# Performance work log

Hardware: AMD Instinct MI355X
Metric: run time of the kernel (lower is better)

The kernel has to match this reference:

```python
import jax, jax.numpy as jnp
import numpy as np

B = 131072      # batch
IN = 1024       # input_dim
H = 384         # hidden[0]
L = 128         # latent_dim = hidden[1]
K = 32          # slots_k
R = 2           # top_r
TAU = 0.7


def setup_inputs() -> dict:
    key = jax.random.key(0)
    ks = jax.random.split(key, 8)
    s = 0.02
    f32 = jnp.float32
    return {
        "x":  jax.random.normal(ks[0], (B, IN), f32),
        "w1": jax.random.normal(ks[1], (IN, H), f32) * s,
        "b1": jnp.zeros((H,), f32),
        "w2": jax.random.normal(ks[2], (H, L), f32) * s,
        "b2": jnp.zeros((L,), f32),
        "mk": jax.random.normal(ks[3], (K, L), f32) * s,  # memory_keys
        "mv": jax.random.normal(ks[4], (K, L), f32) * s,  # memory_values
        "w3": jax.random.normal(ks[5], (2 * L, H), f32) * s,
        "b3": jnp.zeros((H,), f32),
        "w4": jax.random.normal(ks[6], (H, 1), f32) * s,
        "b4": jnp.zeros((1,), f32),
    }


def reference(x, w1, b1, w2, b2, mk, mv, w3, b3, w4, b4):
    # block_a: Linear -> GELU -> (Dropout=id in eval) -> Linear -> GELU
    z = jax.nn.gelu(x @ w1 + b1, approximate=False)
    z = jax.nn.gelu(z @ w2 + b2, approximate=False)          # [B, L]

    # top-r slot attention over memory bank
    logits = (z @ mk.T) / TAU                                 # [B, K]
    _, idx = jax.lax.top_k(logits, R)                         # [B, R]
    keep = jax.nn.one_hot(idx, K, dtype=logits.dtype).sum(-2) > 0  # [B, K] bool
    masked = jnp.where(keep, logits, -jnp.inf)
    attn = jax.nn.softmax(masked, axis=-1)                    # [B, K]
    mem = attn @ mv                                           # [B, L]

    fused = jnp.concatenate([z, mem], axis=-1)                # [B, 2L]

    # default head: Linear -> GELU -> Linear(.,1)
    h = jax.nn.gelu(fused @ w3 + b3, approximate=False)
    logit = (h @ w4 + b4)[..., 0]                             # [B]
    return jax.nn.sigmoid(logit)
```

## Files before the change

### kernel.cpp

```cpp
#include <hip/hip_runtime.h>

#define BATCH   131072
#define INDIM   1024
#define BM      64
#define BDIM    256
#define NBLK    (BATCH / BM)

#define WT0_OFF  0
#define WT1_OFF  24576
#define XTA_OFF  49152
#define XTB_OFF  57344
#define Z1_OFF   0
#define W2T0_OFF 50176
#define W2T1_OFF 58368
#define FZ_OFF   0
#define RP_OFF   33792
#define W3T_OFF  42240
#define CB_OFF   66816
#define B1S_OFF  (CB_OFF)
#define B2S_OFF  (CB_OFF + 1536)
#define B3S_OFF  (CB_OFF + 2048)
#define W4S_OFF  (CB_OFF + 3584)
#define MKS_OFF  (CB_OFF + 5120)
#define SMEM_BYTES (CB_OFF + 13824)

typedef unsigned short u16;
typedef u16    u16x8  __attribute__((ext_vector_type(8)));
typedef u16    u16x4  __attribute__((ext_vector_type(4)));
typedef __bf16 bf16x8 __attribute__((ext_vector_type(8)));
typedef __bf16 bf16x4 __attribute__((ext_vector_type(4)));
typedef float  f32x4  __attribute__((ext_vector_type(4)));

__device__ __forceinline__ u16 f2bf(float f) {
  unsigned u = __float_as_uint(f);
  u += 0x7FFFu + ((u >> 16) & 1u);
  return (u16)(u >> 16);
}

__device__ __forceinline__ float gelu_fast(float v) {
  float t = v * v;
  float u = v * fmaf(t, 0.0356774081f, 0.7978845608f);
  float e = __builtin_amdgcn_exp2f(u * -2.885390082f);
  return v * __builtin_amdgcn_rcpf(1.0f + e);
}

__device__ __forceinline__ f32x4 mfma16(u16x8 a, u16x8 b, f32x4 c) {
  return __builtin_amdgcn_mfma_f32_16x16x32_bf16(
      __builtin_bit_cast(bf16x8, a), __builtin_bit_cast(bf16x8, b), c, 0, 0, 0);
}

__device__ __forceinline__ u16x8 cvt8(float4 a, float4 b) {
  bf16x8 r;
  r[0]=(__bf16)a.x; r[1]=(__bf16)a.y; r[2]=(__bf16)a.z; r[3]=(__bf16)a.w;
  r[4]=(__bf16)b.x; r[5]=(__bf16)b.y; r[6]=(__bf16)b.z; r[7]=(__bf16)b.w;
  return __builtin_bit_cast(u16x8, r);
}
__device__ __forceinline__ u16x4 cvt4(float4 a) {
  bf16x4 r;
  r[0]=(__bf16)a.x; r[1]=(__bf16)a.y; r[2]=(__bf16)a.z; r[3]=(__bf16)a.w;
  return __builtin_bit_cast(u16x4, r);
}

typedef __attribute__((address_space(3))) unsigned int       lds_u32;
typedef __attribute__((address_space(1))) const unsigned int glb_u32;
__device__ __forceinline__ void gload16(const void* g, void* l) {
  __builtin_amdgcn_global_load_lds((glb_u32*)g, (lds_u32*)l, 16, 0, 0);
}

#define FENCE_SCHED __builtin_amdgcn_sched_barrier(0)
#define WAIT_LGKM0 do { asm volatile("s_waitcnt lgkmcnt(0)" ::: "memory"); FENCE_SCHED; } while (0)
#define WAIT_VMN(N) do { asm volatile("s_waitcnt vmcnt(" #N ")" ::: "memory"); FENCE_SCHED; } while (0)
#define BARRIER_LGKM do { \
  asm volatile("s_waitcnt lgkmcnt(0)" ::: "memory"); \
  __builtin_amdgcn_s_barrier(); FENCE_SCHED; } while (0)

__global__ void prep_kernel(const float* __restrict__ w1, const float* __restrict__ w2,
                            const float* __restrict__ w3, u16* __restrict__ w1s,
                            u16* __restrict__ w2s, u16* __restrict__ w3s) {
  int i = blockIdx.x * 256 + threadIdx.x;
  if (i < 393216) {
    int t = i / 12288, p = i % 12288;
    int r = p >> 5, q = p & 31, cp = q >> 3, o = q & 7;
    int k = t * 32 + ((cp ^ ((r >> 1) & 3)) << 3) + o;
    w1s[i] = f2bf(w1[k * 384 + r]);
  } else if (i < 442368) {
    int j = i - 393216;
    int t = j / 4096, p = j % 4096;
    int r = p >> 5, q = p & 31, cp = q >> 3, o = q & 7;
    int k = t * 32 + ((cp ^ ((r >> 1) & 3)) << 3) + o;
    w2s[j] = f2bf(w2[k * 128 + r]);
  } else if (i < 540672) {
    int j = i - 442368;
    int t = j / 12288, p = j % 12288;
    int r = p >> 5, q = p & 31, cp = q >> 3, o = q & 7;
    int k = t * 32 + ((cp ^ ((r >> 1) & 3)) << 3) + o;
    w3s[j] = f2bf(w3[k * 384 + r]);
  }
}

__global__ __launch_bounds__(BDIM, 2) void fused_kernel(
    const float* __restrict__ x,  const u16* __restrict__ w1s,
    const float* __restrict__ b1, const u16* __restrict__ w2s,
    const float* __restrict__ b2, const float* __restrict__ mkw,
    const float* __restrict__ mvw, const u16* __restrict__ w3s,
    const float* __restrict__ b3, const float* __restrict__ w4,
    const float* __restrict__ b4, float* __restrict__ out) {
  extern __shared__ char smem[];
  u16*   z1  = (u16*)(smem + Z1_OFF);
  u16*   fz  = (u16*)(smem + FZ_OFF);
  u16*   w3t = (u16*)(smem + W3T_OFF);
  u16*   wt0 = (u16*)(smem + WT0_OFF);
  u16*   wt1 = (u16*)(smem + WT1_OFF);
  u16*   w2t0 = (u16*)(smem + W2T0_OFF);
  u16*   w2t1 = (u16*)(smem + W2T1_OFF);
  float* b1s = (float*)(smem + B1S_OFF);
  float* b2s = (float*)(smem + B2S_OFF);
  float* b3s = (float*)(smem + B3S_OFF);
  float* w4s = (float*)(smem + W4S_OFF);
  u16*   mks = (u16*)(smem + MKS_OFF);
  float* rowpart = (float*)(smem + RP_OFF);

  const int tid  = threadIdx.x;
  const int lane = tid & 63;
  const int wid  = tid >> 6;
  const int l15  = lane & 15;
  const int g    = lane >> 4;
  const int sw8  = (g ^ ((l15 >> 1) & 3)) * 8;
  const int row0 = blockIdx.x * BM;
  const int wrow = wid * 96;
  const int wstrip = wid * 3072;

  {
    const u16* ws = w1s + wstrip + lane * 8;
    #pragma unroll
    for (int i = 0; i < 6; ++i) gload16(ws + i * 512, wt0 + wstrip + i * 512);
    const u16* ws1 = ws + 12288;
    #pragma unroll
    for (int i = 0; i < 6; ++i) gload16(ws1 + i * 512, wt1 + wstrip + i * 512);
  }
  FENCE_SCHED;
  const int xrow = tid >> 2, xq = tid & 3;
  const float* xp = x + (long)(row0 + xrow) * INDIM + xq * 8;
  const int xpub = xrow * 32 + ((xq ^ ((xrow >> 1) & 3)) << 3);
  float4 xA0 = *(const float4*)xp,        xA1 = *(const float4*)(xp + 4);
  float4 xB0 = *(const float4*)(xp + 32), xB1 = *(const float4*)(xp + 36);

  for (int i = tid; i < 384; i += BDIM) b1s[i] = b1[i];
  if (tid < 128) b2s[tid] = b2[tid];
  for (int i = tid; i < 384; i += BDIM) b3s[i] = b3[i];
  for (int i = tid; i < 384; i += BDIM) w4s[i] = w4[i];
  {
    int r = tid >> 3, cc = (tid & 7) * 16;
    const float4* pm = (const float4*)(mkw + r * 128 + cc);
    *(u16x8*)(mks + r * 136 + cc)     = cvt8(pm[0], pm[1]);
    *(u16x8*)(mks + r * 136 + cc + 8) = cvt8(pm[2], pm[3]);
  }
  *(u16x8*)((u16*)(smem + XTA_OFF) + xpub)        = cvt8(xA0, xA1);
  *(u16x8*)((u16*)(smem + XTA_OFF) + 2048 + xpub) = cvt8(xB0, xB1);
  xA0 = *(const float4*)(xp + 64); xA1 = *(const float4*)(xp + 68);
  xB0 = *(const float4*)(xp + 96); xB1 = *(const float4*)(xp + 100);
  BARRIER_LGKM;

  f32x4 acc[4][6];
  #pragma unroll
  for (int m = 0; m < 4; ++m)
    #pragma unroll
    for (int n = 0; n < 6; ++n) acc[m][n] = (f32x4){0.f, 0.f, 0.f, 0.f};

  for (int p = 0; p < 15; ++p) {
    const u16* xrb = (const u16*)(smem + ((p & 1) ? XTB_OFF : XTA_OFF));
    u16* xwb = (u16*)(smem + ((p & 1) ? XTA_OFF : XTB_OFF));
    WAIT_VMN(10);
    {
      u16x8 af[4], bfr[6];
      #pragma unroll
      for (int m = 0; m < 4; ++m) af[m] = *(const u16x8*)(xrb + (m * 16 + l15) * 32 + sw8);
      #pragma unroll
      for (int n = 0; n < 6; ++n) bfr[n] = *(const u16x8*)(wt0 + (wrow + n * 16 + l15) * 32 + sw8);
      WAIT_LGKM0;
      const u16* ws = w1s + (2 * p + 2) * 12288 + wstrip + lane * 8;
      #pragma unroll
      for (int i = 0; i < 6; ++i) gload16(ws + i * 512, wt0 + wstrip + i * 512);
      #pragma unroll
      for (int m = 0; m < 4; ++m)
        #pragma unroll
        for (int n = 0; n < 6; ++n) acc[m][n] = mfma16(bfr[n], af[m], acc[m][n]);
    }
    WAIT_VMN(10);
    {
      u16x8 af[4], bfr[6];
      #pragma unroll
      for (int m = 0; m < 4; ++m) af[m] = *(const u16x8*)(xrb + 2048 + (m * 16 + l15) * 32 + sw8);
      #pragma unroll
      for (int n = 0; n < 6; ++n) bfr[n] = *(const u16x8*)(wt1 + (wrow + n * 16 + l15) * 32 + sw8);
      WAIT_LGKM0;
      const u16* ws = w1s + (2 * p + 3) * 12288 + wstrip + lane * 8;
      #pragma unroll
      for (int i = 0; i < 6; ++i) gload16(ws + i * 512, wt1 + wstrip + i * 512);
      #pragma unroll
      for (int m = 0; m < 4; ++m)
        #pragma unroll
        for (int n = 0; n < 6; ++n) acc[m][n] = mfma16(bfr[n], af[m], acc[m][n]);
    }
    *(u16x8*)(xwb + xpub)        = cvt8(xA0, xA1);
    *(u16x8*)(xwb + 2048 + xpub) = cvt8(xB0, xB1);
    if (p < 14) {
      xA0 = *(const float4*)(xp + (2 * p + 4) * 32); xA1 = *(const float4*)(xp + (2 * p + 4) * 32 + 4);
      xB0 = *(const float4*)(xp + (2 * p + 5) * 32); xB1 = *(const float4*)(xp + (2 * p + 5) * 32 + 4);
    }
    BARRIER_LGKM;
  }
  {
    const u16* xrb = (const u16*)(smem + XTB_OFF);
    WAIT_VMN(6);
    {
      u16x8 af[4], bfr[6];
      #pragma unroll
      for (int m = 0; m < 4; ++m) af[m] = *(const u16x8*)(xrb + (m * 16 + l15) * 32 + sw8);
      #pragma unroll
      for (int n = 0; n < 6; ++n) bfr[n] = *(const u16x8*)(wt0 + (wrow + n * 16 + l15) * 32 + sw8);
      WAIT_LGKM0;
      #pragma unroll
      for (int m = 0; m < 4; ++m)
        #pragma unroll
        for (int n = 0; n < 6; ++n) acc[m][n] = mfma16(bfr[n], af[m], acc[m][n]);
    }
    WAIT_VMN(0);
    {
      u16x8 af[4], bfr[6];
      #pragma unroll
      for (int m = 0; m < 4; ++m) af[m] = *(const u16x8*)(xrb + 2048 + (m * 16 + l15) * 32 + sw8);
      #pragma unroll
      for (int n = 0; n < 6; ++n) bfr[n] = *(const u16x8*)(wt1 + (wrow + n * 16 + l15) * 32 + sw8);
      WAIT_LGKM0;
      #pragma unroll
      for (int m = 0; m < 4; ++m)
        #pragma unroll
        for (int n = 0; n < 6; ++n) acc[m][n] = mfma16(bfr[n], af[m], acc[m][n]);
    }
  }
  BARRIER_LGKM;

  {
    const u16* s2 = w2s + wid * 1024 + lane * 8;
    gload16(s2, w2t0 + wid * 1024); gload16(s2 + 512, w2t0 + wid * 1024 + 512);
    const u16* s2b = w2s + 4096 + wid * 1024 + lane * 8;
    gload16(s2b, w2t1 + wid * 1024); gload16(s2b + 512, w2t1 + wid * 1024 + 512);
  }
  #pragma unroll
  for (int m = 0; m < 4; ++m) {
    #pragma unroll
    for (int n = 0; n < 6; ++n) {
      int col = wrow + n * 16 + g * 4;
      float4 bv = *(const float4*)(b1s + col);
      f32x4 a = acc[m][n];
      float4 gv = {gelu_fast(a[0] + bv.x), gelu_fast(a[1] + bv.y),
                   gelu_fast(a[2] + bv.z), gelu_fast(a[3] + bv.w)};
      *(u16x4*)(z1 + (m * 16 + l15) * 392 + col) = cvt4(gv);
    }
  }
  BARRIER_LGKM;

  f32x4 acc2[4][2];
  #pragma unroll
  for (int m = 0; m < 4; ++m) { acc2[m][0] = (f32x4){0,0,0,0}; acc2[m][1] = (f32x4){0,0,0,0}; }
  for (int kt = 0; kt < 12; ++kt) {
    if (kt < 11) { WAIT_VMN(2); } else { WAIT_VMN(0); }
    const u16* wb = (kt & 1) ? w2t1 : w2t0;
    u16x8 a2f[4], b2f[2];
    #pragma unroll
    for (int m = 0; m < 4; ++m)
      a2f[m] = *(const u16x8*)(z1 + (m * 16 + l15) * 392 + kt * 32 + g * 8);
    #pragma unroll
    for (int n = 0; n < 2; ++n)
      b2f[n] = *(const u16x8*)(wb + (wid * 32 + n * 16 + l15) * 32 + sw8);
    WAIT_LGKM0;
    if (kt < 10) {
      const u16* s2 = w2s + (kt + 2) * 4096 + wid * 1024 + lane * 8;
      u16* d2 = ((kt & 1) ? w2t1 : w2t0) + wid * 1024;
      gload16(s2, d2); gload16(s2 + 512, d2 + 512);
    }
    #pragma unroll
    for (int m = 0; m < 4; ++m)
      #pragma unroll
      for (int n = 0; n < 2; ++n) acc2[m][n] = mfma16(b2f[n], a2f[m], acc2[m][n]);
  }
  BARRIER_LGKM;

  {
    const u16* s3 = w3s + wstrip + lane * 8;
    #pragma unroll
    for (int i = 0; i < 6; ++i) gload16(s3 + i * 512, w3t + wstrip + i * 512);
  }
  #pragma unroll
  for (int m = 0; m < 4; ++m) {
    #pragma unroll
    for (int n = 0; n < 2; ++n) {
      int col = wid * 32 + n * 16 + g * 4;
      float4 bv = *(const float4*)(b2s + col);
      f32x4 a = acc2[m][n];
      float4 gv = {gelu_fast(a[0] + bv.x), gelu_fast(a[1] + bv.y),
                   gelu_fast(a[2] + bv.z), gelu_fast(a[3] + bv.w)};
      *(u16x4*)(fz + (m * 16 + l15) * 264 + col) = cvt4(gv);
    }
  }
  BARRIER_LGKM;

  {
    const int wr = wid * 16 + l15;
    f32x4 accl[2] = {(f32x4){0,0,0,0}, (f32x4){0,0,0,0}};
    #pragma unroll
    for (int ks = 0; ks < 4; ++ks) {
      u16x8 afz = *(const u16x8*)(fz + wr * 264 + ks * 32 + g * 8);
      u16x8 k0  = *(const u16x8*)(mks + l15 * 136 + ks * 32 + g * 8);
      u16x8 k1  = *(const u16x8*)(mks + (16 + l15) * 136 + ks * 32 + g * 8);
      accl[0] = mfma16(k0, afz, accl[0]);
      accl[1] = mfma16(k1, afz, accl[1]);
    }
    float m1 = -3.4e38f, m2 = -3.4e38f; int i1 = -1, i2 = -1;
    #pragma unroll
    for (int n = 0; n < 2; ++n)
      #pragma unroll
      for (int j = 0; j < 4; ++j) {
        float v = accl[n][j]; int idx = n * 16 + g * 4 + j;
        if (v > m1) { m2 = m1; i2 = i1; m1 = v; i1 = idx; }
        else if (v > m2) { m2 = v; i2 = idx; }
      }
    #pragma unroll
    for (int d = 16; d <= 32; d <<= 1) {
      float om1 = __shfl_xor(m1, d); int oi1 = __shfl_xor(i1, d);
      float om2 = __shfl_xor(m2, d); int oi2 = __shfl_xor(i2, d);
      bool take = (om1 > m1) || (om1 == m1 && oi1 < i1);
      if (take) {
        float nm2; int ni2;
        if (m1 > om2 || (m1 == om2 && i1 < oi2)) { nm2 = m1; ni2 = i1; }
        else { nm2 = om2; ni2 = oi2; }
        m1 = om1; i1 = oi1; m2 = nm2; i2 = ni2;
      } else {
        if (om1 > m2 || (om1 == m2 && oi1 < i2)) { m2 = om1; i2 = oi1; }
      }
    }
    float a1 = __builtin_amdgcn_rcpf(
        1.0f + __builtin_amdgcn_exp2f((m2 - m1) * (1.44269504f / 0.7f)));
    float a2 = 1.0f - a1;
    const float* v1 = mvw + i1 * 128 + g * 32;
    const float* v2 = mvw + i2 * 128 + g * 32;
    #pragma unroll
    for (int c = 0; c < 4; ++c) {
      float4 A0 = *(const float4*)(v1 + c * 8), A1 = *(const float4*)(v1 + c * 8 + 4);
      float4 B0 = *(const float4*)(v2 + c * 8), B1 = *(const float4*)(v2 + c * 8 + 4);
      float4 r0 = {a1*A0.x + a2*B0.x, a1*A0.y + a2*B0.y, a1*A0.z + a2*B0.z, a1*A0.w + a2*B0.w};
      float4 r1 = {a1*A1.x + a2*B1.x, a1*A1.y + a2*B1.y, a1*A1.z + a2*B1.z, a1*A1.w + a2*B1.w};
      *(u16x8*)(fz + wr * 264 + 128 + g * 32 + c * 8) = cvt8(r0, r1);
    }
  }
  BARRIER_LGKM;

  f32x4 acc3[4][6];
  #pragma unroll
  for (int m = 0; m < 4; ++m)
    #pragma unroll
    for (int n = 0; n < 6; ++n) acc3[m][n] = (f32x4){0.f, 0.f, 0.f, 0.f};
  for (int kt = 0; kt < 8; ++kt) {
    WAIT_VMN(0);
    u16x8 a3f[4], b3f[6];
    #pragma unroll
    for (int m = 0; m < 4; ++m)
      a3f[m] = *(const u16x8*)(fz + (m * 16 + l15) * 264 + kt * 32 + g * 8);
    #pragma unroll
    for (int n = 0; n < 6; ++n)
      b3f[n] = *(const u16x8*)(w3t + (wrow + n * 16 + l15) * 32 + sw8);
    WAIT_LGKM0;
    if (kt < 7) {
      const u16* s3 = w3s + (kt + 1) * 12288 + wstrip + lane * 8;
      #pragma unroll
      for (int i = 0; i < 6; ++i) gload16(s3 + i * 512, w3t + wstrip + i * 512);
    }
    #pragma unroll
    for (int m = 0; m < 4; ++m)
      #pragma unroll
      for (int n = 0; n < 6; ++n) acc3[m][n] = mfma16(b3f[n], a3f[m], acc3[m][n]);
  }

  #pragma unroll
  for (int m = 0; m < 4; ++m) {
    float s = 0.f;
    #pragma unroll
    for (int n = 0; n < 6; ++n) {
      int col = wrow + n * 16 + g * 4;
      float4 bv = *(const float4*)(b3s + col);
      float4 wv = *(const float4*)(w4s + col);
      f32x4 a = acc3[m][n];
      s += gelu_fast(a[0] + bv.x) * wv.x + gelu_fast(a[1] + bv.y) * wv.y +
           gelu_fast(a[2] + bv.z) * wv.z + gelu_fast(a[3] + bv.w) * wv.w;
    }
    s += __shfl_xor(s, 16);
    s += __shfl_xor(s, 32);
    if (lane < 16) rowpart[(m * 16 + l15) * 4 + wid] = s;
  }
  BARRIER_LGKM;
  if (tid < BM) {
    const float4* rp = (const float4*)(rowpart + tid * 4);
    float4 p0 = rp[0];
    float lg = b4[0] + p0.x + p0.y + p0.z + p0.w;
    out[row0 + tid] = __builtin_amdgcn_rcpf(1.0f + __builtin_amdgcn_exp2f(-lg * 1.44269504f));
  }
}

extern "C" void kernel_launch(void* const* d_in, const int* in_sizes, int n_in,
                              void* d_out, int out_size, void* d_ws, size_t ws_size,
                              hipStream_t stream) {
  const float* x  = (const float*)d_in[0];
  const float* w1 = (const float*)d_in[1];
  const float* b1 = (const float*)d_in[2];
  const float* w2 = (const float*)d_in[3];
  const float* b2 = (const float*)d_in[4];
  const float* mk = (const float*)d_in[5];
  const float* mv = (const float*)d_in[6];
  const float* w3 = (const float*)d_in[7];
  const float* b3 = (const float*)d_in[8];
  const float* w4 = (const float*)d_in[9];
  const float* b4 = (const float*)d_in[10];

  u16* w1s = (u16*)d_ws;
  u16* w2s = w1s + 393216;
  u16* w3s = w1s + 442368;

  prep_kernel<<<2112, 256, 0, stream>>>(w1, w2, w3, w1s, w2s, w3s);

  (void)hipFuncSetAttribute(reinterpret_cast<const void*>(fused_kernel),
                            hipFuncAttributeMaxDynamicSharedMemorySize, SMEM_BYTES);
  fused_kernel<<<NBLK, BDIM, SMEM_BYTES, stream>>>(x, w1s, b1, w2s, b2, mk, mv, w3s,
                                                   b3, w4, b4, (float*)d_out);
}
```

Measured before the change: 237.4 us.

## Merge GEMM1 half-steps and drop scheduling barriers around waitcnts

Restructures the first GEMM loop so both K-halves' LDS fragments are read up front. The first MFMA batch runs, then weight prefetches for both next tiles are issued together and the second MFMA batch is placed after the x conversion store. The vmcnt threshold is adjusted to match the single combined wait, and the sched_barrier fences are removed from the wait macros so the compiler can interleave work. The aim is fewer wait points and better overlap of LDS reads, global-to-LDS copies and MFMAs, at the cost of more live fragment registers and weaker scheduling control.

```diff
diff --git a/kernel.cpp b/kernel.cpp
--- a/kernel.cpp
+++ b/kernel.cpp
@@ -67,12 +67,12 @@
   __builtin_amdgcn_global_load_lds((glb_u32*)g, (lds_u32*)l, 16, 0, 0);
 }
 
-#define FENCE_SCHED __builtin_amdgcn_sched_barrier(0)
-#define WAIT_LGKM0 do { asm volatile("s_waitcnt lgkmcnt(0)" ::: "memory"); FENCE_SCHED; } while (0)
-#define WAIT_VMN(N) do { asm volatile("s_waitcnt vmcnt(" #N ")" ::: "memory"); FENCE_SCHED; } while (0)
+#define SOFT_LGKM0 asm volatile("s_waitcnt lgkmcnt(0)" ::: "memory")
+#define SOFT_VMN(N) asm volatile("s_waitcnt vmcnt(" #N ")" ::: "memory")
 #define BARRIER_LGKM do { \
   asm volatile("s_waitcnt lgkmcnt(0)" ::: "memory"); \
-  __builtin_amdgcn_s_barrier(); FENCE_SCHED; } while (0)
+  __builtin_amdgcn_s_barrier(); \
+  __builtin_amdgcn_sched_barrier(0); } while (0)
 
 __global__ void prep_kernel(const float* __restrict__ w1, const float* __restrict__ w2,
                             const float* __restrict__ w3, u16* __restrict__ w1s,
@@ -138,7 +138,6 @@
     #pragma unroll
     for (int i = 0; i < 6; ++i) gload16(ws1 + i * 512, wt1 + wstrip + i * 512);
   }
-  FENCE_SCHED;
   const int xrow = tid >> 2, xq = tid & 3;
   const float* xp = x + (long)(row0 + xrow) * INDIM + xq * 8;
   const int xpub = xrow * 32 + ((xq ^ ((xrow >> 1) & 3)) << 3);
@@ -170,37 +169,28 @@
   for (int p = 0; p < 15; ++p) {
     const u16* xrb = (const u16*)(smem + ((p & 1) ? XTB_OFF : XTA_OFF));
     u16* xwb = (u16*)(smem + ((p & 1) ? XTA_OFF : XTB_OFF));
-    WAIT_VMN(10);
+    SOFT_VMN(4);
+    u16x8 af0[4], bf0[6], af1[4], bf1[6];
+    #pragma unroll
+    for (int m = 0; m < 4; ++m) af0[m] = *(const u16x8*)(xrb + (m * 16 + l15) * 32 + sw8);
+    #pragma unroll
+    for (int n = 0; n < 6; ++n) bf0[n] = *(const u16x8*)(wt0 + (wrow + n * 16 + l15) * 32 + sw8);
+    #pragma unroll
+    for (int m = 0; m < 4; ++m) af1[m] = *(const u16x8*)(xrb + 2048 + (m * 16 + l15) * 32 + sw8);
+    #pragma unroll
+    for (int n = 0; n < 6; ++n) bf1[n] = *(const u16x8*)(wt1 + (wrow + n * 16 + l15) * 32 + sw8);
+    #pragma unroll
+    for (int m = 0; m < 4; ++m)
+      #pragma unroll
+      for (int n = 0; n < 6; ++n) acc[m][n] = mfma16(bf0[n], af0[m], acc[m][n]);
+    SOFT_LGKM0;
     {
-      u16x8 af[4], bfr[6];
-      #pragma unroll
-      for (int m = 0; m < 4; ++m) af[m] = *(const u16x8*)(xrb + (m * 16 + l15) * 32 + sw8);
-      #pragma unroll
-      for (int n = 0; n < 6; ++n) bfr[n] = *(const u16x8*)(wt0 + (wrow + n * 16 + l15) * 32 + sw8);
-      WAIT_LGKM0;
-      const u16* ws = w1s + (2 * p + 2) * 12288 + wstrip + lane * 8;
-      #pragma unroll
-      for (int i = 0; i < 6; ++i) gload16(ws + i * 512, wt0 + wstrip + i * 512);
-      #pragma unroll
-      for (int m = 0; m < 4; ++m)
-        #pragma unroll
-        for (int n = 0; n < 6; ++n) acc[m][n] = mfma16(bfr[n], af[m], acc[m][n]);
-    }
-    WAIT_VMN(10);
-    {
-      u16x8 af[4], bfr[6];
-      #pragma unroll
-      for (int m = 0; m < 4; ++m) af[m] = *(const u16x8*)(xrb + 2048 + (m * 16 + l15) * 32 + sw8);
-      #pragma unroll
-      for (int n = 0; n < 6; ++n) bfr[n] = *(const u16x8*)(wt1 + (wrow + n * 16 + l15) * 32 + sw8);
-      WAIT_LGKM0;
-      const u16* ws = w1s + (2 * p + 3) * 12288 + wstrip + lane * 8;
-      #pragma unroll
-      for (int i = 0; i < 6; ++i) gload16(ws + i * 512, wt1 + wstrip + i * 512);
-      #pragma unroll
-      for (int m = 0; m < 4; ++m)
-        #pragma unroll
-        for (int n = 0; n < 6; ++n) acc[m][n] = mfma16(bfr[n], af[m], acc[m][n]);
+      const u16* ws0 = w1s + (2 * p + 2) * 12288 + wstrip + lane * 8;
+      #pragma unroll
+      for (int i = 0; i < 6; ++i) gload16(ws0 + i * 512, wt0 + wstrip + i * 512);
+      const u16* ws1 = w1s + (2 * p + 3) * 12288 + wstrip + lane * 8;
+      #pragma unroll
+      for (int i = 0; i < 6; ++i) gload16(ws1 + i * 512, wt1 + wstrip + i * 512);
     }
     *(u16x8*)(xwb + xpub)        = cvt8(xA0, xA1);
     *(u16x8*)(xwb + 2048 + xpub) = cvt8(xB0, xB1);
@@ -208,36 +198,32 @@
       xA0 = *(const float4*)(xp + (2 * p + 4) * 32); xA1 = *(const float4*)(xp + (2 * p + 4) * 32 + 4);
       xB0 = *(const float4*)(xp + (2 * p + 5) * 32); xB1 = *(const float4*)(xp + (2 * p + 5) * 32 + 4);
     }
+    #pragma unroll
+    for (int m = 0; m < 4; ++m)
+      #pragma unroll
+      for (int n = 0; n < 6; ++n) acc[m][n] = mfma16(bf1[n], af1[m], acc[m][n]);
     BARRIER_LGKM;
   }
   {
     const u16* xrb = (const u16*)(smem + XTB_OFF);
-    WAIT_VMN(6);
-    {
-      u16x8 af[4], bfr[6];
-      #pragma unroll
-      for (int m = 0; m < 4; ++m) af[m] = *(const u16x8*)(xrb + (m * 16 + l15) * 32 + sw8);
-      #pragma unroll
-      for (int n = 0; n < 6; ++n) bfr[n] = *(const u16x8*)(wt0 + (wrow + n * 16 + l15) * 32 + sw8);
-      WAIT_LGKM0;
-      #pragma unroll
-      for (int m = 0; m < 4; ++m)
-        #pragma unroll
-        for (int n = 0; n < 6; ++n) acc[m][n] = mfma16(bfr[n], af[m], acc[m][n]);
-    }
-    WAIT_VMN(0);
-    {
-      u16x8 af[4], bfr[6];
-      #pragma unroll
-      for (int m = 0; m < 4; ++m) af[m] = *(const u16x8*)(xrb + 2048 + (m * 16 + l15) * 32 + sw8);
-      #pragma unroll
-      for (int n = 0; n < 6; ++n) bfr[n] = *(const u16x8*)(wt1 + (wrow + n * 16 + l15) * 32 + sw8);
-      WAIT_LGKM0;
-      #pragma unroll
-      for (int m = 0; m < 4; ++m)
-        #pragma unroll
-        for (int n = 0; n < 6; ++n) acc[m][n] = mfma16(bfr[n], af[m], acc[m][n]);
-    }
+    SOFT_VMN(0);
+    u16x8 af0[4], bf0[6], af1[4], bf1[6];
+    #pragma unroll
+    for (int m = 0; m < 4; ++m) af0[m] = *(const u16x8*)(xrb + (m * 16 + l15) * 32 + sw8);
+    #pragma unroll
+    for (int n = 0; n < 6; ++n) bf0[n] = *(const u16x8*)(wt0 + (wrow + n * 16 + l15) * 32 + sw8);
+    #pragma unroll
+    for (int m = 0; m < 4; ++m) af1[m] = *(const u16x8*)(xrb + 2048 + (m * 16 + l15) * 32 + sw8);
+    #pragma unroll
+    for (int n = 0; n < 6; ++n) bf1[n] = *(const u16x8*)(wt1 + (wrow + n * 16 + l15) * 32 + sw8);
+    #pragma unroll
+    for (int m = 0; m < 4; ++m)
+      #pragma unroll
+      for (int n = 0; n < 6; ++n) acc[m][n] = mfma16(bf0[n], af0[m], acc[m][n]);
+    #pragma unroll
+    for (int m = 0; m < 4; ++m)
+      #pragma unroll
+      for (int n = 0; n < 6; ++n) acc[m][n] = mfma16(bf1[n], af1[m], acc[m][n]);
   }
   BARRIER_LGKM;
 
@@ -265,7 +251,7 @@
   #pragma unroll
   for (int m = 0; m < 4; ++m) { acc2[m][0] = (f32x4){0,0,0,0}; acc2[m][1] = (f32x4){0,0,0,0}; }
   for (int kt = 0; kt < 12; ++kt) {
-    if (kt < 11) { WAIT_VMN(2); } else { WAIT_VMN(0); }
+    if (kt < 11) { SOFT_VMN(2); } else { SOFT_VMN(0); }
     const u16* wb = (kt & 1) ? w2t1 : w2t0;
     u16x8 a2f[4], b2f[2];
     #pragma unroll
@@ -274,7 +260,7 @@
     #pragma unroll
     for (int n = 0; n < 2; ++n)
       b2f[n] = *(const u16x8*)(wb + (wid * 32 + n * 16 + l15) * 32 + sw8);
-    WAIT_LGKM0;
+    SOFT_LGKM0;
     if (kt < 10) {
       const u16* s2 = w2s + (kt + 2) * 4096 + wid * 1024 + lane * 8;
       u16* d2 = ((kt & 1) ? w2t1 : w2t0) + wid * 1024;
@@ -362,7 +348,7 @@
     #pragma unroll
     for (int n = 0; n < 6; ++n) acc3[m][n] = (f32x4){0.f, 0.f, 0.f, 0.f};
   for (int kt = 0; kt < 8; ++kt) {
-    WAIT_VMN(0);
+    SOFT_VMN(0);
     u16x8 a3f[4], b3f[6];
     #pragma unroll
     for (int m = 0; m < 4; ++m)
@@ -370,7 +356,7 @@
     #pragma unroll
     for (int n = 0; n < 6; ++n)
       b3f[n] = *(const u16x8*)(w3t + (wrow + n * 16 + l15) * 32 + sw8);
-    WAIT_LGKM0;
+    SOFT_LGKM0;
     if (kt < 7) {
       const u16* s3 = w3s + (kt + 1) * 12288 + wstrip + lane * 8;
       #pragma unroll
```

Measured after the change: 259.3 us. 9.2% more time.
